# Kernel optimization log

Measured on AMD Instinct MI355X. Metric: run time of the kernel, lower is better.

Reference implementation:

```python
import jax, jax.numpy as jnp
import numpy as np

B, C, H, W = 8, 256, 128, 128
BN_EPS = 1e-5

def setup_inputs() -> dict:
    key = jax.random.key(0)
    ks = jax.random.split(key, 7)
    scale = 1.0 / np.sqrt(C)
    x = jax.random.normal(ks[0], (B, C, H, W), dtype=jnp.float32)
    w_qkv = jax.random.normal(ks[1], (3 * C, C), dtype=jnp.float32) * scale
    w_proj = jax.random.normal(ks[2], (C, C), dtype=jnp.float32) * scale
    gamma = jax.random.uniform(ks[3], (C,), dtype=jnp.float32)
    beta = jax.random.normal(ks[4], (C,), dtype=jnp.float32)
    running_mean = jax.random.normal(ks[5], (C,), dtype=jnp.float32)
    running_var = jax.random.uniform(ks[6], (C,), dtype=jnp.float32) + 0.5
    return {"x": x, "w_qkv": w_qkv, "w_proj": w_proj, "gamma": gamma,
            "beta": beta, "running_mean": running_mean, "running_var": running_var}

def reference(x, w_qkv, w_proj, gamma, beta, running_mean, running_var):
    b, c, h, w = x.shape
    n = h * w
    xf = x.reshape(b, c, n)                       # flatten spatial
    # 1x1 conv == channel matmul: [3c,c] x [b,c,n] -> [b,3c,n]
    qkv = jnp.einsum('oc,bcn->bon', w_qkv, xf)
    q, k, v = jnp.split(qkv, 3, axis=1)           # each [b,c,n]
    k = jax.nn.softmax(k, axis=-1)                # softmax over spatial
    context = jnp.einsum('bcn,bdn->bcd', k, v)    # k @ v^T, [b,c,c]
    out = jnp.einsum('bcd,bcn->bdn', context, q)  # context^T @ q, [b,c,n]
    out = jnp.einsum('oc,bcn->bon', w_proj, out)  # 1x1 proj
    # BatchNorm (inference form with running stats)
    inv = gamma / jnp.sqrt(running_var + BN_EPS)
    out = out * inv[None, :, None] + (beta - running_mean * inv)[None, :, None]
    out = jax.nn.relu(out)
    return out.reshape(b, c, h, w)
```

## Files before the change

kernel.cpp:

```cpp
#include <hip/hip_runtime.h>
#include <stdint.h>

#define B_   8
#define C_   256
#define N_   16384

#define NS    32
#define KVP   40

typedef __attribute__((ext_vector_type(8))) short bf16x8;
typedef __attribute__((ext_vector_type(4))) float f32x4;

__device__ inline float bf2f(unsigned short h) {
    return __uint_as_float(((unsigned)h) << 16);
}
__device__ inline unsigned short f2bf(float f) {
    unsigned u = __float_as_uint(f);
    u += 0x7FFF + ((u >> 16) & 1);
    return (unsigned short)(u >> 16);
}
__device__ inline unsigned cvt_pk_bf16(float lo, float hi) {
    unsigned r;
    asm("v_cvt_pk_bf16_f32 %0, %1, %2" : "=v"(r) : "v"(lo), "v"(hi));
    return r;
}

__device__ inline void gl_lds16(const void* g, void* l) {
    __builtin_amdgcn_global_load_lds(
        reinterpret_cast<const __attribute__((address_space(1))) unsigned int*>(
            reinterpret_cast<uintptr_t>(g)),
        reinterpret_cast<__attribute__((address_space(3))) unsigned int*>(
            reinterpret_cast<uintptr_t>(l)),
        16, 0, 0);
}

__device__ inline f32x4 mfma16(bf16x8 a, bf16x8 b, f32x4 c) {
    return __builtin_amdgcn_mfma_f32_16x16x32_bf16(a, b, c, 0, 0, 0);
}

__global__ __launch_bounds__(256) void k1_transpose(const float* __restrict__ x,
                                                    unsigned short* __restrict__ xT) {
    __shared__ unsigned short tile[64][65];
    const int b = blockIdx.z, c0 = blockIdx.y * 64, n0 = blockIdx.x * 64;
    const float* xb = x + (size_t)b * C_ * N_;
    const int t = threadIdx.x;
    const int tr = t >> 4, tc4 = (t & 15) * 4;
#pragma unroll
    for (int p = 0; p < 4; p++) {
        const int i = p * 16 + tr;
        const float4 v = *(const float4*)(xb + (size_t)(c0 + i) * N_ + n0 + tc4);
        tile[i][tc4 + 0] = f2bf(v.x);
        tile[i][tc4 + 1] = f2bf(v.y);
        tile[i][tc4 + 2] = f2bf(v.z);
        tile[i][tc4 + 3] = f2bf(v.w);
    }
    __syncthreads();
    unsigned short* xTb = xT + (size_t)b * N_ * C_;
#pragma unroll
    for (int p = 0; p < 4; p++) {
        const int jj = p * 16 + tr;
        ushort4 o;
        o.x = tile[tc4 + 0][jj];
        o.y = tile[tc4 + 1][jj];
        o.z = tile[tc4 + 2][jj];
        o.w = tile[tc4 + 3][jj];
        *(ushort4*)(xTb + (size_t)(n0 + jj) * C_ + c0 + tc4) = o;
    }
}

__global__ __launch_bounds__(256) void k1b_setup(const float* __restrict__ wqkv,
                                                 const float* __restrict__ gamma,
                                                 const float* __restrict__ beta,
                                                 const float* __restrict__ rmean,
                                                 const float* __restrict__ rvar,
                                                 unsigned short* __restrict__ WkvF,
                                                 float* __restrict__ inv,
                                                 float* __restrict__ b2,
                                                 float* __restrict__ rsum) {
    const int t = threadIdx.x;
    if (blockIdx.x < 64) {
        const int chunk = blockIdx.x * 256 + t;
        const int lane = chunk & 63;
        const int kb = (chunk >> 6) & 7;
        const int rb = chunk >> 9;
        const int row = rb * 16 + (lane & 15);
        const int k0 = kb * 32 + (lane >> 4) * 8;
        const float* src = wqkv + (size_t)(256 + row) * 256 + k0;
        const float4 a = *(const float4*)(src);
        const float4 c = *(const float4*)(src + 4);
        ushort4 o0, o1;
        o0.x = f2bf(a.x); o0.y = f2bf(a.y); o0.z = f2bf(a.z); o0.w = f2bf(a.w);
        o1.x = f2bf(c.x); o1.y = f2bf(c.y); o1.z = f2bf(c.z); o1.w = f2bf(c.w);
        *(ushort4*)(WkvF + (size_t)chunk * 8) = o0;
        *(ushort4*)(WkvF + (size_t)chunk * 8 + 4) = o1;
    } else {
        const float iv = gamma[t] * rsqrtf(rvar[t] + 1e-5f);
        inv[t] = iv;
        b2[t]  = beta[t] - rmean[t] * iv;
        float4 z = {0.f, 0.f, 0.f, 0.f};
        *(float4*)(rsum + t * 8)     = z;
        *(float4*)(rsum + t * 8 + 4) = z;
    }
}

__global__ __launch_bounds__(512, 2) void k2_ctx(const unsigned short* __restrict__ WkvF,
                                                 const unsigned short* __restrict__ xT,
                                                 float* __restrict__ cp,
                                                 float* __restrict__ rsum) {
    __shared__ __align__(16) unsigned short xs[2][NS * 256];
    __shared__ __align__(16) unsigned short kvs[384 * KVP];
    const int chunk = blockIdx.x;
    const int h  = blockIdx.y;
    const int b  = blockIdx.z;
    const int n0 = chunk * 512;
    const int t = threadIdx.x, wave = t >> 6, lane = t & 63;
    const int fr = lane & 15, fkq = lane >> 4;
    const int wr = wave >> 1, wc = wave & 1;
    const unsigned short* xTb = xT + (size_t)b * N_ * C_;

    bf16x8 wf[3][8];
    {
        const int rbs[3] = {wave, 8 + wave, 16 + h * 8 + wave};
#pragma unroll
        for (int slot = 0; slot < 3; slot++)
#pragma unroll
            for (int kb = 0; kb < 8; kb++)
                wf[slot][kb] = *(const bf16x8*)(
                    WkvF + (((size_t)rbs[slot] * 8 + kb) * 64 + lane) * 8);
    }
    const int rowbase[3] = {wave * 16, 128 + wave * 16, 256 + wave * 16};

    f32x4 acc[4][4];
#pragma unroll
    for (int i = 0; i < 4; i++)
#pragma unroll
        for (int j = 0; j < 4; j++)
#pragma unroll
            for (int r = 0; r < 4; r++) acc[i][j][r] = 0.f;
    float rsacc[2] = {0.f, 0.f};

    auto stage = [&](int buf, int sc) {
        const int nb = n0 + sc * NS;
#pragma unroll
        for (int it = 0; it < 2; it++) {
            const int idx = it * 512 + t;
            const int r = idx >> 5;
            const int c = (idx & 31) * 8;
            const int csw = c ^ ((r & 7) * 8);
            gl_lds16(xTb + (size_t)(nb + r) * 256 + csw,
                     &xs[buf][it * 4096 + wave * 512]);
        }
    };

    stage(0, 0);
    __syncthreads();

    for (int s = 0; s < 16; ++s) {
        const int cur = s & 1;
        if (s < 15) stage(cur ^ 1, s + 1);

        f32x4 kacc[3][2];
#pragma unroll
        for (int i = 0; i < 3; i++)
#pragma unroll
            for (int j = 0; j < 2; j++)
#pragma unroll
                for (int r = 0; r < 4; r++) kacc[i][j][r] = 0.f;
#pragma unroll
        for (int kb = 0; kb < 8; kb++) {
            bf16x8 bfa[2];
#pragma unroll
            for (int jj = 0; jj < 2; jj++) {
                const int rr = jj * 16 + fr;
                const int cs = (kb * 32 + fkq * 8) ^ ((fr & 7) * 8);
                bfa[jj] = *(const bf16x8*)(&xs[cur][rr * 256 + cs]);
            }
#pragma unroll
            for (int slot = 0; slot < 3; slot++) {
                kacc[slot][0] = mfma16(bfa[0], wf[slot][kb], kacc[slot][0]);
                kacc[slot][1] = mfma16(bfa[1], wf[slot][kb], kacc[slot][1]);
            }
        }
#pragma unroll
        for (int slot = 0; slot < 3; slot++) {
            const int kvrow = rowbase[slot] + fr;
#pragma unroll
            for (int jj = 0; jj < 2; jj++) {
                f32x4 v = kacc[slot][jj];
                if (slot < 2) {
                    v[0] = __expf(v[0]); v[1] = __expf(v[1]);
                    v[2] = __expf(v[2]); v[3] = __expf(v[3]);
                    rsacc[slot] += (v[0] + v[1]) + (v[2] + v[3]);
                }
                uint2 pk;
                pk.x = cvt_pk_bf16(v[0], v[1]);
                pk.y = cvt_pk_bf16(v[2], v[3]);
                *(uint2*)(&kvs[kvrow * KVP + jj * 16 + fkq * 4]) = pk;
            }
        }
        __syncthreads();

        {
            bf16x8 a2[4], b2v[4];
#pragma unroll
            for (int i = 0; i < 4; i++) {
                const int row = wr * 64 + i * 16 + fr;
                a2[i] = *(const bf16x8*)(&kvs[row * KVP + fkq * 8]);
            }
#pragma unroll
            for (int j = 0; j < 4; j++) {
                const int row = 256 + wc * 64 + j * 16 + fr;
                b2v[j] = *(const bf16x8*)(&kvs[row * KVP + fkq * 8]);
            }
#pragma unroll
            for (int i = 0; i < 4; i++)
#pragma unroll
                for (int j = 0; j < 4; j++)
                    acc[i][j] = mfma16(a2[i], b2v[j], acc[i][j]);
        }
        __syncthreads();
    }

    float* cpb = cp + ((size_t)((b * 2 + h) * 32 + chunk)) * 256 * 128;
#pragma unroll
    for (int i = 0; i < 4; i++) {
        const int gc = wr * 64 + i * 16 + fkq * 4;
#pragma unroll
        for (int j = 0; j < 4; j++) {
            const int gd = wc * 64 + j * 16 + fr;
#pragma unroll
            for (int r = 0; r < 4; r++)
                cpb[(size_t)(gc + r) * 128 + gd] = acc[i][j][r];
        }
    }
    if (h == 0) {
#pragma unroll
        for (int slot = 0; slot < 2; slot++) {
            float sv = rsacc[slot];
            sv += __shfl_xor(sv, 16, 64);
            sv += __shfl_xor(sv, 32, 64);
            if (fkq == 0)
                atomicAdd(&rsum[b * 256 + slot * 128 + wave * 16 + fr], sv);
        }
    }
}

__global__ __launch_bounds__(256) void k4r_reduce(const float* __restrict__ cp,
                                                  float* __restrict__ ctx) {
    const int gid = blockIdx.x * 256 + threadIdx.x;
    const int d4 = gid & 31;
    const int c  = (gid >> 5) & 255;
    const int h  = (gid >> 13) & 1;
    const int b  = gid >> 14;
    const float* src = cp + ((size_t)((b * 2 + h) * 32) * 256 + c) * 128 + d4 * 4;
    f32x4 s = {0.f, 0.f, 0.f, 0.f};
#pragma unroll
    for (int k = 0; k < 32; k++)
        s = s + *(const f32x4*)(src + (size_t)k * 32768);
    *(f32x4*)(ctx + ((size_t)b * 256 + c) * 256 + h * 128 + d4 * 4) = s;
}

__global__ __launch_bounds__(256) void k5a_T(const float* __restrict__ Wp,
                                             const float* __restrict__ ctx,
                                             const float* __restrict__ rsum,
                                             float* __restrict__ T) {
    __shared__ float Asm[64][65];
    __shared__ float Bsm[64][65];
    const int b = blockIdx.z;
    const int o0 = blockIdx.y * 64, c0 = blockIdx.x * 64;
    const int t = threadIdx.x;
    const int tm = t >> 4, tn = t & 15;
    const int lc4 = tn * 4;
    float acc[4][4] = {};
    const float* cb = ctx + (size_t)b * C_ * C_;
    for (int kk = 0; kk < 256; kk += 64) {
        __syncthreads();
#pragma unroll
        for (int p = 0; p < 4; p++) {
            const int r = p * 16 + tm;
            const float4 av = *(const float4*)(Wp + (size_t)(o0 + r) * C_ + kk + lc4);
            Asm[r][lc4] = av.x; Asm[r][lc4 + 1] = av.y; Asm[r][lc4 + 2] = av.z; Asm[r][lc4 + 3] = av.w;
            const float4 bv = *(const float4*)(cb + (size_t)(c0 + r) * C_ + kk + lc4);
            Bsm[r][lc4] = bv.x; Bsm[r][lc4 + 1] = bv.y; Bsm[r][lc4 + 2] = bv.z; Bsm[r][lc4 + 3] = bv.w;
        }
        __syncthreads();
        for (int k = 0; k < 64; k++) {
            float a_[4], b_[4];
#pragma unroll
            for (int i = 0; i < 4; i++) a_[i] = Asm[tm * 4 + i][k];
#pragma unroll
            for (int j = 0; j < 4; j++) b_[j] = Bsm[tn * 4 + j][k];
#pragma unroll
            for (int i = 0; i < 4; i++)
#pragma unroll
                for (int j = 0; j < 4; j++) acc[i][j] += a_[i] * b_[j];
        }
    }
    float isv[4];
#pragma unroll
    for (int j = 0; j < 4; j++) isv[j] = 1.f / rsum[b * 256 + c0 + tn * 4 + j];
#pragma unroll
    for (int i = 0; i < 4; i++)
#pragma unroll
        for (int j = 0; j < 4; j++)
            T[((size_t)b * C_ + o0 + tm * 4 + i) * C_ + c0 + tn * 4 + j] = acc[i][j] * isv[j];
}

__global__ __launch_bounds__(256) void k5b_G(const float* __restrict__ Tm,
                                             const float* __restrict__ Wq,
                                             const float* __restrict__ inv,
                                             unsigned short* __restrict__ G) {
    __shared__ float Asm[64][65];
    __shared__ float Bsm[64][65];
    const int b = blockIdx.z;
    const int o0 = blockIdx.y * 64, j0 = blockIdx.x * 64;
    const int t = threadIdx.x;
    const int tm = t >> 4, tn = t & 15;
    const int lc4 = tn * 4;
    float acc[4][4] = {};
    const float* Tb = Tm + (size_t)b * C_ * C_;
    for (int kk = 0; kk < 256; kk += 64) {
        __syncthreads();
#pragma unroll
        for (int p = 0; p < 4; p++) {
            const int r = p * 16 + tm;
            const float4 av = *(const float4*)(Tb + (size_t)(o0 + r) * C_ + kk + lc4);
            Asm[r][lc4] = av.x; Asm[r][lc4 + 1] = av.y; Asm[r][lc4 + 2] = av.z; Asm[r][lc4 + 3] = av.w;
            const float4 bv = *(const float4*)(Wq + (size_t)(kk + r) * C_ + j0 + lc4);
            Bsm[r][lc4] = bv.x; Bsm[r][lc4 + 1] = bv.y; Bsm[r][lc4 + 2] = bv.z; Bsm[r][lc4 + 3] = bv.w;
        }
        __syncthreads();
        for (int k = 0; k < 64; k++) {
            float a_[4], b_[4];
#pragma unroll
            for (int i = 0; i < 4; i++) a_[i] = Asm[tm * 4 + i][k];
#pragma unroll
            for (int j = 0; j < 4; j++) b_[j] = Bsm[k][tn * 4 + j];
#pragma unroll
            for (int i = 0; i < 4; i++)
#pragma unroll
                for (int j = 0; j < 4; j++) acc[i][j] += a_[i] * b_[j];
        }
    }
#pragma unroll
    for (int i = 0; i < 4; i++) {
        const float iv = inv[o0 + tm * 4 + i];
#pragma unroll
        for (int j = 0; j < 4; j++)
            G[((size_t)b * C_ + o0 + tm * 4 + i) * C_ + j0 + tn * 4 + j] = f2bf(acc[i][j] * iv);
    }
}

__global__ __launch_bounds__(256) void k6_out(const unsigned short* __restrict__ G,
                                              const unsigned short* __restrict__ xT,
                                              const float* __restrict__ b2,
                                              float* __restrict__ out) {
    __shared__ __align__(16) unsigned short As[128 * 32];
    __shared__ __align__(16) unsigned short Bs[128 * 32];
    const int b  = blockIdx.z;
    const int m0 = blockIdx.y * 128;
    const int n0 = blockIdx.x * 128;
    const int t = threadIdx.x, wave = t >> 6, lane = t & 63;
    const int wm = wave >> 1, wn = wave & 1;

    const unsigned short* Gb  = G  + (size_t)b * C_ * C_;
    const unsigned short* xTb = xT + (size_t)b * N_ * C_;

    const int ch1 = wave * 64 + lane, ch2 = ch1 + 256;
    const int r1 = ch1 >> 2, q1 = ch1 & 3;
    const int r2 = ch2 >> 2, q2 = ch2 & 3;
    unsigned short* ldsA1 = As + wave * 512;
    unsigned short* ldsA2 = As + 2048 + wave * 512;
    unsigned short* ldsB1 = Bs + wave * 512;
    unsigned short* ldsB2 = Bs + 2048 + wave * 512;

    f32x4 acc[4][4];
#pragma unroll
    for (int i = 0; i < 4; i++)
#pragma unroll
        for (int j = 0; j < 4; j++)
#pragma unroll
            for (int r = 0; r < 4; r++) acc[i][j][r] = 0.f;

    const int fr = lane & 15;
    const int fk = (lane >> 4) * 8;

    for (int kk = 0; kk < 256; kk += 32) {
        __syncthreads();
        gl_lds16(Gb  + (size_t)(m0 + r1) * 256 + kk + q1 * 8, ldsA1);
        gl_lds16(Gb  + (size_t)(m0 + r2) * 256 + kk + q2 * 8, ldsA2);
        gl_lds16(xTb + (size_t)(n0 + r1) * 256 + kk + q1 * 8, ldsB1);
        gl_lds16(xTb + (size_t)(n0 + r2) * 256 + kk + q2 * 8, ldsB2);
        __syncthreads();
        bf16x8 af[4], bfv[4];
#pragma unroll
        for (int i = 0; i < 4; i++)
            af[i] = *(const bf16x8*)(As + (wm * 64 + i * 16 + fr) * 32 + fk);
#pragma unroll
        for (int j = 0; j < 4; j++)
            bfv[j] = *(const bf16x8*)(Bs + (wn * 64 + j * 16 + fr) * 32 + fk);
#pragma unroll
        for (int i = 0; i < 4; i++)
#pragma unroll
            for (int j = 0; j < 4; j++)
                acc[i][j] = mfma16(af[i], bfv[j], acc[i][j]);
    }

    const int col = lane & 15, rowq = (lane >> 4) * 4;
    float* ob = out + (size_t)b * C_ * N_;
#pragma unroll
    for (int i = 0; i < 4; i++) {
        const int gm = m0 + wm * 64 + i * 16 + rowq;
#pragma unroll
        for (int j = 0; j < 4; j++) {
            const int gn = n0 + wn * 64 + j * 16 + col;
#pragma unroll
            for (int r = 0; r < 4; r++) {
                const float val = fmaxf(acc[i][j][r] + b2[gm + r], 0.f);
                ob[(size_t)(gm + r) * N_ + gn] = val;
            }
        }
    }
}

extern "C" void kernel_launch(void* const* d_in, const int* in_sizes, int n_in,
                              void* d_out, int out_size, void* d_ws, size_t ws_size,
                              hipStream_t stream) {
    const float* x     = (const float*)d_in[0];
    const float* wqkv  = (const float*)d_in[1];
    const float* wproj = (const float*)d_in[2];
    const float* gamma = (const float*)d_in[3];
    const float* beta  = (const float*)d_in[4];
    const float* rmean = (const float*)d_in[5];
    const float* rvar  = (const float*)d_in[6];
    float* out = (float*)d_out;

    char* ws = (char*)d_ws;
    size_t off = 0;
    auto alloc = [&](size_t bytes) {
        void* p = ws + off;
        off += (bytes + 255) & ~(size_t)255;
        return p;
    };
    unsigned short* xT   = (unsigned short*)alloc((size_t)B_ * N_ * C_ * 2);
    unsigned short* WkvF = (unsigned short*)alloc((size_t)512 * 256 * 2);
    float* invp = (float*)alloc(256 * 4);
    float* b2p  = (float*)alloc(256 * 4);
    float* cp   = (float*)alloc((size_t)512 * 256 * 128 * 4);
    float* ctx  = (float*)alloc((size_t)B_ * C_ * C_ * 4);
    float* rsum = (float*)alloc(2048 * 4);
    float* Tm   = (float*)alloc((size_t)B_ * C_ * C_ * 4);
    unsigned short* G = (unsigned short*)alloc((size_t)B_ * C_ * C_ * 2);

    hipLaunchKernelGGL(k1_transpose, dim3(256, 4, 8), dim3(256), 0, stream, x, xT);
    hipLaunchKernelGGL(k1b_setup, dim3(65), dim3(256), 0, stream,
                       wqkv, gamma, beta, rmean, rvar, WkvF, invp, b2p, rsum);
    hipLaunchKernelGGL(k2_ctx, dim3(32, 2, 8), dim3(512), 0, stream, WkvF, xT, cp, rsum);
    hipLaunchKernelGGL(k4r_reduce, dim3(512), dim3(256), 0, stream, cp, ctx);
    hipLaunchKernelGGL(k5a_T, dim3(4, 4, 8), dim3(256), 0, stream, wproj, ctx, rsum, Tm);
    hipLaunchKernelGGL(k5b_G, dim3(4, 4, 8), dim3(256), 0, stream, Tm, wqkv, invp, G);
    hipLaunchKernelGGL(k6_out, dim3(128, 2, 8), dim3(256), 0, stream, G, xT, b2p, out);
}
```

Before: 381.5 us.

## Reduce context partials with float atomics and use nontemporal loads/stores

The separate partial-context buffer and its reduction kernel are removed. Each k2_ctx block now atomically adds its 256x128 tile into a zero-initialised ctx, which the setup kernel clears using 512 extra blocks. The large x read in the transpose and the final output write use nontemporal loads/stores to limit cache pollution. This saves writing and re-reading about 64 MB of partials and one launch, at the cost of 32-way atomic contention per element and a sum order that is no longer deterministic.

```diff
diff --git a/kernel.cpp b/kernel.cpp
--- a/kernel.cpp
+++ b/kernel.cpp
@@ -48,11 +48,12 @@
 #pragma unroll
     for (int p = 0; p < 4; p++) {
         const int i = p * 16 + tr;
-        const float4 v = *(const float4*)(xb + (size_t)(c0 + i) * N_ + n0 + tc4);
-        tile[i][tc4 + 0] = f2bf(v.x);
-        tile[i][tc4 + 1] = f2bf(v.y);
-        tile[i][tc4 + 2] = f2bf(v.z);
-        tile[i][tc4 + 3] = f2bf(v.w);
+        const f32x4 v = __builtin_nontemporal_load(
+            (const f32x4*)(xb + (size_t)(c0 + i) * N_ + n0 + tc4));
+        tile[i][tc4 + 0] = f2bf(v[0]);
+        tile[i][tc4 + 1] = f2bf(v[1]);
+        tile[i][tc4 + 2] = f2bf(v[2]);
+        tile[i][tc4 + 3] = f2bf(v[3]);
     }
     __syncthreads();
     unsigned short* xTb = xT + (size_t)b * N_ * C_;
@@ -76,7 +77,8 @@
                                                  unsigned short* __restrict__ WkvF,
                                                  float* __restrict__ inv,
                                                  float* __restrict__ b2,
-                                                 float* __restrict__ rsum) {
+                                                 float* __restrict__ rsum,
+                                                 float* __restrict__ ctx) {
     const int t = threadIdx.x;
     if (blockIdx.x < 64) {
         const int chunk = blockIdx.x * 256 + t;
@@ -93,19 +95,23 @@
         o1.x = f2bf(c.x); o1.y = f2bf(c.y); o1.z = f2bf(c.z); o1.w = f2bf(c.w);
         *(ushort4*)(WkvF + (size_t)chunk * 8) = o0;
         *(ushort4*)(WkvF + (size_t)chunk * 8 + 4) = o1;
-    } else {
+    } else if (blockIdx.x == 64) {
         const float iv = gamma[t] * rsqrtf(rvar[t] + 1e-5f);
         inv[t] = iv;
         b2[t]  = beta[t] - rmean[t] * iv;
         float4 z = {0.f, 0.f, 0.f, 0.f};
         *(float4*)(rsum + t * 8)     = z;
         *(float4*)(rsum + t * 8 + 4) = z;
+    } else {
+        const int idx = (blockIdx.x - 65) * 256 + t;
+        float4 z = {0.f, 0.f, 0.f, 0.f};
+        *(float4*)(ctx + (size_t)idx * 4) = z;
     }
 }
 
 __global__ __launch_bounds__(512, 2) void k2_ctx(const unsigned short* __restrict__ WkvF,
                                                  const unsigned short* __restrict__ xT,
-                                                 float* __restrict__ cp,
+                                                 float* __restrict__ ctx,
                                                  float* __restrict__ rsum) {
     __shared__ __align__(16) unsigned short xs[2][NS * 256];
     __shared__ __align__(16) unsigned short kvs[384 * KVP];
@@ -221,7 +227,7 @@
         __syncthreads();
     }
 
-    float* cpb = cp + ((size_t)((b * 2 + h) * 32 + chunk)) * 256 * 128;
+    float* cb = ctx + (size_t)b * C_ * C_ + h * 128;
 #pragma unroll
     for (int i = 0; i < 4; i++) {
         const int gc = wr * 64 + i * 16 + fkq * 4;
@@ -230,7 +236,7 @@
             const int gd = wc * 64 + j * 16 + fr;
 #pragma unroll
             for (int r = 0; r < 4; r++)
-                cpb[(size_t)(gc + r) * 128 + gd] = acc[i][j][r];
+                atomicAdd(&cb[(size_t)(gc + r) * C_ + gd], acc[i][j][r]);
         }
     }
     if (h == 0) {
@@ -243,21 +249,6 @@
                 atomicAdd(&rsum[b * 256 + slot * 128 + wave * 16 + fr], sv);
         }
     }
-}
-
-__global__ __launch_bounds__(256) void k4r_reduce(const float* __restrict__ cp,
-                                                  float* __restrict__ ctx) {
-    const int gid = blockIdx.x * 256 + threadIdx.x;
-    const int d4 = gid & 31;
-    const int c  = (gid >> 5) & 255;
-    const int h  = (gid >> 13) & 1;
-    const int b  = gid >> 14;
-    const float* src = cp + ((size_t)((b * 2 + h) * 32) * 256 + c) * 128 + d4 * 4;
-    f32x4 s = {0.f, 0.f, 0.f, 0.f};
-#pragma unroll
-    for (int k = 0; k < 32; k++)
-        s = s + *(const f32x4*)(src + (size_t)k * 32768);
-    *(f32x4*)(ctx + ((size_t)b * 256 + c) * 256 + h * 128 + d4 * 4) = s;
 }
 
 __global__ __launch_bounds__(256) void k5a_T(const float* __restrict__ Wp,
@@ -417,7 +408,7 @@
 #pragma unroll
             for (int r = 0; r < 4; r++) {
                 const float val = fmaxf(acc[i][j][r] + b2[gm + r], 0.f);
-                ob[(size_t)(gm + r) * N_ + gn] = val;
+                __builtin_nontemporal_store(val, &ob[(size_t)(gm + r) * N_ + gn]);
             }
         }
     }
@@ -446,17 +437,15 @@
     unsigned short* WkvF = (unsigned short*)alloc((size_t)512 * 256 * 2);
     float* invp = (float*)alloc(256 * 4);
     float* b2p  = (float*)alloc(256 * 4);
-    float* cp   = (float*)alloc((size_t)512 * 256 * 128 * 4);
     float* ctx  = (float*)alloc((size_t)B_ * C_ * C_ * 4);
     float* rsum = (float*)alloc(2048 * 4);
     float* Tm   = (float*)alloc((size_t)B_ * C_ * C_ * 4);
     unsigned short* G = (unsigned short*)alloc((size_t)B_ * C_ * C_ * 2);
 
     hipLaunchKernelGGL(k1_transpose, dim3(256, 4, 8), dim3(256), 0, stream, x, xT);
-    hipLaunchKernelGGL(k1b_setup, dim3(65), dim3(256), 0, stream,
-                       wqkv, gamma, beta, rmean, rvar, WkvF, invp, b2p, rsum);
-    hipLaunchKernelGGL(k2_ctx, dim3(32, 2, 8), dim3(512), 0, stream, WkvF, xT, cp, rsum);
-    hipLaunchKernelGGL(k4r_reduce, dim3(512), dim3(256), 0, stream, cp, ctx);
+    hipLaunchKernelGGL(k1b_setup, dim3(577), dim3(256), 0, stream,
+                       wqkv, gamma, beta, rmean, rvar, WkvF, invp, b2p, rsum, ctx);
+    hipLaunchKernelGGL(k2_ctx, dim3(32, 2, 8), dim3(512), 0, stream, WkvF, xT, ctx, rsum);
     hipLaunchKernelGGL(k5a_T, dim3(4, 4, 8), dim3(256), 0, stream, wproj, ctx, rsum, Tm);
     hipLaunchKernelGGL(k5b_G, dim3(4, 4, 8), dim3(256), 0, stream, Tm, wqkv, invp, G);
     hipLaunchKernelGGL(k6_out, dim3(128, 2, 8), dim3(256), 0, stream, G, xT, b2p, out);
```

After: 406.9 us. 6.6% more time.
